# Kernel optimization log

Hardware: AMD Instinct MI355X
Metric: run time of the kernel (lower is better)

The kernel has to match this reference:

```python
import jax, jax.numpy as jnp
import numpy as np

B, C, L = 8, 512, 4096
CK, CV = C // 8, C // 2  # 64, 256


def maxpool2(t):
    # max_pool1d(kernel=2, stride=2) over last axis: [B, c, L] -> [B, c, L//2]
    b, c, l = t.shape
    return t.reshape(b, c, l // 2, 2).max(axis=-1)


def setup_inputs() -> dict:
    key = jax.random.key(0)
    ks = jax.random.split(key, 6)
    return {
        "x": jax.random.normal(ks[0], (B, C, L), dtype=jnp.float32),
        "W_theta": jax.random.normal(ks[1], (CK, C), dtype=jnp.float32) * 0.02,
        "W_phi": jax.random.normal(ks[2], (CK, C), dtype=jnp.float32) * 0.02,
        "W_g": jax.random.normal(ks[3], (CV, C), dtype=jnp.float32) * 0.02,
        "W_o": jax.random.normal(ks[4], (C, CV), dtype=jnp.float32) * 0.02,
        "gamma": jax.random.normal(ks[5], (), dtype=jnp.float32),
    }


def reference(x, W_theta, W_phi, W_g, W_o, gamma):
    # 1x1 convs are channel matmuls
    theta = jnp.einsum("kc,bcl->bkl", W_theta, x)            # [B, C/8, L]
    phi = maxpool2(jnp.einsum("kc,bcl->bkl", W_phi, x))      # [B, C/8, L/2]
    g = maxpool2(jnp.einsum("vc,bcl->bvl", W_g, x))          # [B, C/2, L/2]
    # attention scores over downsampled keys: [B, L, L/2]
    scores = jnp.einsum("bkl,bkm->blm", theta, phi)
    beta = jax.nn.softmax(scores, axis=-1)
    # aggregate values: g @ beta^T -> [B, C/2, L]
    o_in = jnp.einsum("bvm,blm->bvl", g, beta)
    o = jnp.einsum("ov,bvl->bol", W_o, o_in)                 # [B, C, L]
    return gamma * o + x
```

## Files before the change

kernel.cpp:

```cpp
#include <hip/hip_runtime.h>
#include <cstdint>
#include <cstddef>

#define B_ 8
#define C_ 512
#define L_ 4096
#define M_ 2048
#define CK_ 64
#define CV_ 256

typedef _Float16 f16;
typedef _Float16 f16x8 __attribute__((ext_vector_type(8)));
typedef _Float16 f16x4 __attribute__((ext_vector_type(4)));
typedef float f32x4 __attribute__((ext_vector_type(4)));
typedef float f32x16 __attribute__((ext_vector_type(16)));
typedef unsigned int u32x4 __attribute__((ext_vector_type(4)));

#define MFMA16(A, Bv, Cv) __builtin_amdgcn_mfma_f32_16x16x32_f16(A, Bv, Cv, 0, 0, 0)
#define MFMA32(A, Bv, Cv) __builtin_amdgcn_mfma_f32_32x32x16_f16(A, Bv, Cv, 0, 0, 0)

#define LOG2E 1.44269504f

static __device__ __forceinline__ uint32_t pkrtz(float a, float b) {
    return __builtin_bit_cast(uint32_t, __builtin_amdgcn_cvt_pkrtz(a, b));
}

__global__ __launch_bounds__(256) void cvt_all(const float* __restrict__ Wt,
                                               const float* __restrict__ Wp,
                                               const float* __restrict__ Wg,
                                               const float* __restrict__ Wo,
                                               f16* __restrict__ WallF,
                                               f16* __restrict__ WoF) {
    const int i = blockIdx.x * 256 + threadIdx.x;
    const int NW = 384 * 512;
    if (i < NW) {
        const int och = i >> 9, c = i & 511;
        float v;
        if (och < 64)       v = Wt[i];
        else if (och < 128) v = Wp[i - 64 * 512];
        else                v = Wg[i - 128 * 512];
        const int idx = (((och >> 4) * 16 + (c >> 5)) * 64 +
                         (((c >> 3) & 3) << 4) + (och & 15)) * 8 + (c & 7);
        WallF[idx] = (f16)v;
    } else {
        const int j = i - NW;
        const int oc = j >> 8, v = j & 255;
        const int idx = (((oc >> 4) * 8 + (v >> 5)) * 64 +
                         (((v >> 3) & 3) << 4) + (oc & 15)) * 8 + (v & 7);
        WoF[idx] = (f16)Wo[j];
    }
}

__global__ __launch_bounds__(256) void fused_proj(const f16* __restrict__ WallF,
                                                  const float* __restrict__ x,
                                                  f16* __restrict__ theta2,
                                                  f16* __restrict__ phi2,
                                                  f16* __restrict__ g2) {
    __shared__ __align__(16) f16 xs[64][32][8];
    const int b    = blockIdx.y;
    const int l0   = blockIdx.x * 32;
    const int tid  = threadIdx.x;
    const int w    = tid >> 6;
    const int lane = tid & 63;
    const int lq   = lane & 15;
    const int g    = lane >> 4;
    const int wb   = w * 96;

    {
        const float* xb = x + (size_t)b * C_ * L_ + l0 + (tid & 31);
        const int co0 = tid >> 5;
#pragma unroll
        for (int i = 0; i < 8; ++i) {
            const int co = i * 8 + co0;
            float v[8];
#pragma unroll
            for (int j = 0; j < 8; ++j) v[j] = xb[(size_t)(co * 8 + j) * L_];
            u32x4 p = {pkrtz(v[0], v[1]), pkrtz(v[2], v[3]),
                       pkrtz(v[4], v[5]), pkrtz(v[6], v[7])};
            *reinterpret_cast<u32x4*>(&xs[co][tid & 31][0]) = p;
        }
    }
    __syncthreads();

    f32x4 acc[6][2] = {};
    for (int ks = 0; ks < 16; ++ks) {
        f16x8 Bf[2];
#pragma unroll
        for (int lt = 0; lt < 2; ++lt)
            Bf[lt] = *reinterpret_cast<const f16x8*>(&xs[ks * 4 + g][lt * 16 + lq][0]);
#pragma unroll
        for (int t = 0; t < 6; ++t) {
            f16x8 Af = *reinterpret_cast<const f16x8*>(
                WallF + (((size_t)(6 * w + t) * 16 + ks) * 64 + lane) * 8);
            acc[t][0] = MFMA16(Af, Bf[0], acc[t][0]);
            acc[t][1] = MFMA16(Af, Bf[1], acc[t][1]);
        }
    }

#pragma unroll
    for (int t = 0; t < 6; ++t) {
        const int och0 = wb + t * 16;
#pragma unroll
        for (int lt = 0; lt < 2; ++lt) {
            const int l = l0 + lt * 16 + lq;
            if (och0 < 64) {
#pragma unroll
                for (int r = 0; r < 4; ++r) {
                    const int och = och0 + 4 * g + r;
                    theta2[(((size_t)b * 8 + (och >> 3)) * L_ + l) * 8 + (och & 7)] =
                        (f16)(acc[t][lt][r] * LOG2E);
                }
            } else {
#pragma unroll
                for (int r = 0; r < 4; ++r) {
                    const float pv = fmaxf(acc[t][lt][r], __shfl_xor(acc[t][lt][r], 1));
                    if (!(lane & 1)) {
                        const int m = l >> 1;
                        if (och0 < 128) {
                            const int kc = och0 - 64 + 4 * g + r;
                            phi2[(((size_t)b * 8 + (kc >> 3)) * M_ + m) * 8 + (kc & 7)] =
                                (f16)pv;
                        } else {
                            const int vc = och0 - 128 + 4 * g + r;
                            g2[(((size_t)b * 256 + (m >> 3)) * CV_ + vc) * 8 + (m & 7)] =
                                (f16)pv;
                        }
                    }
                }
            }
        }
    }
}

__global__ __launch_bounds__(512, 4) void attn_flash(const f16* __restrict__ theta2,
                                                     const f16* __restrict__ phi2,
                                                     const f16* __restrict__ g2,
                                                     f16* __restrict__ o2) {
    const int bid = blockIdx.x;
    const int b   = bid & 7;
    const int qt  = bid >> 3;
    const int w   = threadIdx.x >> 6;
    const int qg  = w >> 2;
    const int vq  = w & 3;
    const int q0  = qt * 64 + qg * 32;
    const int vb  = vq * 64;
    const int lane = threadIdx.x & 63;
    const int lq   = lane & 31;
    const int hi   = lane >> 5;

    const f16* qbase = theta2 + (size_t)b * 8 * L_ * 8;
    f16x8 Qf[4];
#pragma unroll
    for (int f = 0; f < 4; ++f)
        Qf[f] = *reinterpret_cast<const f16x8*>(
            qbase + ((size_t)(2 * f + hi) * L_ + q0 + lq) * 8);

    f32x16 acc[2] = {};
    float m_run = -3.0e38f;
    float l_run = 0.f;

    const f16* kbase = phi2 + (size_t)b * 8 * M_ * 8;
    const f16* vbase = g2 + (size_t)b * 256 * CV_ * 8;

    uint32_t ko[4], vo[4];
#pragma unroll
    for (int f = 0; f < 4; ++f) ko[f] = ((2 * f + hi) * M_ + lq) * 8u;
#pragma unroll
    for (int ch = 0; ch < 2; ++ch)
#pragma unroll
        for (int vt = 0; vt < 2; ++vt)
            vo[ch * 2 + vt] = ((2 * ch + hi) * CV_ + vb + vt * 32 + lq) * 8u;

    for (int m0 = 0; m0 < M_; m0 += 32) {
        f16x8 Kf[4];
#pragma unroll
        for (int f = 0; f < 4; ++f)
            Kf[f] = *reinterpret_cast<const f16x8*>(kbase + ko[f]);
        f16x8 Vf[2][2];
#pragma unroll
        for (int ch = 0; ch < 2; ++ch)
#pragma unroll
            for (int vt = 0; vt < 2; ++vt)
                Vf[ch][vt] = *reinterpret_cast<const f16x8*>(vbase + vo[ch * 2 + vt]);

        f32x16 S = {};
        __builtin_amdgcn_s_setprio(1);
#pragma unroll
        for (int f = 0; f < 4; ++f) S = MFMA32(Kf[f], Qf[f], S);
        __builtin_amdgcn_s_setprio(0);

        float t0 = fmaxf(fmaxf(S[0], S[1]), S[2]);
        float t1 = fmaxf(fmaxf(S[3], S[4]), S[5]);
        float t2 = fmaxf(fmaxf(S[6], S[7]), S[8]);
        float t3 = fmaxf(fmaxf(S[9], S[10]), S[11]);
        float t4 = fmaxf(fmaxf(S[12], S[13]), S[14]);
        float tm = fmaxf(fmaxf(fmaxf(t0, t1), t2),
                         fmaxf(fmaxf(t3, t4), S[15]));
        tm = fmaxf(tm, __shfl_xor(tm, 32));
        if (__any(tm > m_run + 11.5f)) {
            const float m_new = fmaxf(m_run, tm);
            const float sc = __builtin_amdgcn_exp2f(m_run - m_new);
#pragma unroll
            for (int vt = 0; vt < 2; ++vt)
#pragma unroll
                for (int r = 0; r < 16; ++r) acc[vt][r] *= sc;
            l_run *= sc;
            m_run = m_new;
        }
        float s[16];
#pragma unroll
        for (int r = 0; r < 16; ++r) s[r] = __builtin_amdgcn_exp2f(S[r] - m_run);
        float a0 = (s[0] + s[1]) + (s[2] + s[3]);
        float a1 = (s[4] + s[5]) + (s[6] + s[7]);
        float a2 = (s[8] + s[9]) + (s[10] + s[11]);
        float a3 = (s[12] + s[13]) + (s[14] + s[15]);
        l_run += (a0 + a1) + (a2 + a3);

        uint32_t pk[8];
#pragma unroll
        for (int i = 0; i < 8; ++i) pk[i] = pkrtz(s[2 * i], s[2 * i + 1]);
        asm volatile("v_permlane32_swap_b32 %0, %1" : "+v"(pk[0]), "+v"(pk[2]));
        asm volatile("v_permlane32_swap_b32 %0, %1" : "+v"(pk[1]), "+v"(pk[3]));
        asm volatile("v_permlane32_swap_b32 %0, %1" : "+v"(pk[4]), "+v"(pk[6]));
        asm volatile("v_permlane32_swap_b32 %0, %1" : "+v"(pk[5]), "+v"(pk[7]));
        u32x4 fr0 = {pk[0], pk[1], pk[2], pk[3]};
        u32x4 fr1 = {pk[4], pk[5], pk[6], pk[7]};
        f16x8 P0 = __builtin_bit_cast(f16x8, fr0);
        f16x8 P1 = __builtin_bit_cast(f16x8, fr1);

        __builtin_amdgcn_s_setprio(1);
#pragma unroll
        for (int vt = 0; vt < 2; ++vt) acc[vt] = MFMA32(Vf[0][vt], P0, acc[vt]);
#pragma unroll
        for (int vt = 0; vt < 2; ++vt) acc[vt] = MFMA32(Vf[1][vt], P1, acc[vt]);
        __builtin_amdgcn_s_setprio(0);

#pragma unroll
        for (int f = 0; f < 4; ++f) ko[f] += 32u * 8u;
#pragma unroll
        for (int i = 0; i < 4; ++i) vo[i] += 4u * CV_ * 8u;
    }

    l_run += __shfl_xor(l_run, 32);
    const float inv = 1.f / l_run;
    const int qtile = (q0 >> 4) + (lq >> 4);
    const int ql    = lq & 15;
#pragma unroll
    for (int vt = 0; vt < 2; ++vt)
#pragma unroll
        for (int rq = 0; rq < 4; ++rq) {
            f16x4 o;
#pragma unroll
            for (int j = 0; j < 4; ++j) o[j] = (f16)(acc[vt][4 * rq + j] * inv);
            f16* p = o2 + ((((size_t)b * 256 + qtile) * 8 + vq * 2 + vt) * 64 +
                           rq * 16 + ql) * 8 + 4 * hi;
            *reinterpret_cast<f16x4*>(p) = o;
        }
}

__global__ __launch_bounds__(256) void out_mfma(const f16* __restrict__ WoF,
                                                const f16* __restrict__ o2,
                                                const float* __restrict__ x,
                                                const float* __restrict__ gamma_p,
                                                float* __restrict__ out) {
    const int b    = blockIdx.z;
    const int l0   = blockIdx.x * 64;
    const int wid  = threadIdx.x >> 6;
    const int oc0  = blockIdx.y * 64 + wid * 16;
    const int lane = threadIdx.x & 63;
    const int lq   = lane & 15;
    const int g    = lane >> 4;

    f32x4 acc[4] = {{0.f, 0.f, 0.f, 0.f}, {0.f, 0.f, 0.f, 0.f},
                    {0.f, 0.f, 0.f, 0.f}, {0.f, 0.f, 0.f, 0.f}};
#pragma unroll
    for (int ks = 0; ks < 8; ++ks) {
        f16x8 A = *reinterpret_cast<const f16x8*>(
            WoF + (((size_t)(oc0 >> 4) * 8 + ks) * 64 + lane) * 8);
#pragma unroll
        for (int lt = 0; lt < 4; ++lt) {
            const f16* bp = o2 + (((size_t)(b * 256 + (l0 >> 4) + lt) * 8 + ks) * 64 +
                                  lane) * 8;
            acc[lt] = MFMA16(A, *reinterpret_cast<const f16x8*>(bp), acc[lt]);
        }
    }
    const float gamma = *gamma_p;
#pragma unroll
    for (int lt = 0; lt < 4; ++lt)
#pragma unroll
        for (int r = 0; r < 4; ++r) {
            const size_t o = ((size_t)b * C_ + oc0 + 4 * g + r) * L_ + l0 + lt * 16 + lq;
            out[o] = fmaf(gamma, acc[lt][r], x[o]);
        }
}

extern "C" void kernel_launch(void* const* d_in, const int* in_sizes, int n_in,
                              void* d_out, int out_size, void* d_ws, size_t ws_size,
                              hipStream_t stream) {
    const float* x       = (const float*)d_in[0];
    const float* W_theta = (const float*)d_in[1];
    const float* W_phi   = (const float*)d_in[2];
    const float* W_g     = (const float*)d_in[3];
    const float* W_o     = (const float*)d_in[4];
    const float* gamma   = (const float*)d_in[5];
    float* out = (float*)d_out;

    f16* theta2 = (f16*)d_ws;
    f16* phi2   = theta2 + (size_t)B_ * 8 * L_ * 8;
    f16* g2     = phi2 + (size_t)B_ * 8 * M_ * 8;
    f16* o2     = g2 + (size_t)B_ * 256 * CV_ * 8;
    f16* WoF    = o2 + (size_t)B_ * L_ * CV_;
    f16* WallF  = WoF + (size_t)C_ * CV_;

    const int cvt_n = 384 * 512 + 512 * 256;
    cvt_all<<<dim3(cvt_n / 256), 256, 0, stream>>>(W_theta, W_phi, W_g, W_o, WallF, WoF);
    fused_proj<<<dim3(L_ / 32, B_), 256, 0, stream>>>(WallF, x, theta2, phi2, g2);
    attn_flash<<<dim3(512), 512, 0, stream>>>(theta2, phi2, g2, o2);
    out_mfma<<<dim3(L_ / 64, C_ / 64, B_), 256, 0, stream>>>(WoF, o2, x, gamma, out);
}
```

Baseline: 176.9 us.

## Split attention key range across wave pairs and merge partial softmax via LDS

```diff
diff --git a/kernel.cpp b/kernel.cpp
--- a/kernel.cpp
+++ b/kernel.cpp
@@ -12,6 +12,7 @@
 typedef _Float16 f16;
 typedef _Float16 f16x8 __attribute__((ext_vector_type(8)));
 typedef _Float16 f16x4 __attribute__((ext_vector_type(4)));
+typedef _Float16 f16x2 __attribute__((ext_vector_type(2)));
 typedef float f32x4 __attribute__((ext_vector_type(4)));
 typedef float f32x16 __attribute__((ext_vector_type(16)));
 typedef unsigned int u32x4 __attribute__((ext_vector_type(4)));
@@ -136,14 +137,17 @@
                                                      const f16* __restrict__ phi2,
                                                      const f16* __restrict__ g2,
                                                      f16* __restrict__ o2) {
+    __shared__ uint32_t lds_o[2][2][64][33];
+    __shared__ float lds_ml[2][2][2][64];
     const int bid = blockIdx.x;
     const int b   = bid & 7;
     const int qt  = bid >> 3;
     const int w   = threadIdx.x >> 6;
     const int qg  = w >> 2;
-    const int vq  = w & 3;
+    const int vq  = (w >> 1) & 1;
+    const int mh  = w & 1;
     const int q0  = qt * 64 + qg * 32;
-    const int vb  = vq * 64;
+    const int vb  = vq * 128;
     const int lane = threadIdx.x & 63;
     const int lq   = lane & 31;
     const int hi   = lane >> 5;
@@ -155,33 +159,32 @@
         Qf[f] = *reinterpret_cast<const f16x8*>(
             qbase + ((size_t)(2 * f + hi) * L_ + q0 + lq) * 8);
 
-    f32x16 acc[2] = {};
+    f32x16 acc[4] = {};
     float m_run = -3.0e38f;
     float l_run = 0.f;
 
     const f16* kbase = phi2 + (size_t)b * 8 * M_ * 8;
     const f16* vbase = g2 + (size_t)b * 256 * CV_ * 8;
 
-    uint32_t ko[4], vo[4];
-#pragma unroll
-    for (int f = 0; f < 4; ++f) ko[f] = ((2 * f + hi) * M_ + lq) * 8u;
+    uint32_t ko[4], vo[2];
+#pragma unroll
+    for (int f = 0; f < 4; ++f) ko[f] = ((2 * f + hi) * M_ + mh * 1024 + lq) * 8u;
 #pragma unroll
     for (int ch = 0; ch < 2; ++ch)
-#pragma unroll
-        for (int vt = 0; vt < 2; ++vt)
-            vo[ch * 2 + vt] = ((2 * ch + hi) * CV_ + vb + vt * 32 + lq) * 8u;
-
-    for (int m0 = 0; m0 < M_; m0 += 32) {
+        vo[ch] = ((mh * 128 + 2 * ch + hi) * CV_ + vb + lq) * 8u;
+
+    for (int it = 0; it < 32; ++it) {
         f16x8 Kf[4];
 #pragma unroll
         for (int f = 0; f < 4; ++f)
             Kf[f] = *reinterpret_cast<const f16x8*>(kbase + ko[f]);
-        f16x8 Vf[2][2];
+        f16x8 Vf[2][4];
 #pragma unroll
         for (int ch = 0; ch < 2; ++ch)
 #pragma unroll
-            for (int vt = 0; vt < 2; ++vt)
-                Vf[ch][vt] = *reinterpret_cast<const f16x8*>(vbase + vo[ch * 2 + vt]);
+            for (int vt = 0; vt < 4; ++vt)
+                Vf[ch][vt] = *reinterpret_cast<const f16x8*>(
+                    vbase + vo[ch] + vt * 32 * 8);
 
         f32x16 S = {};
         __builtin_amdgcn_s_setprio(1);
@@ -201,7 +204,7 @@
             const float m_new = fmaxf(m_run, tm);
             const float sc = __builtin_amdgcn_exp2f(m_run - m_new);
 #pragma unroll
-            for (int vt = 0; vt < 2; ++vt)
+            for (int vt = 0; vt < 4; ++vt)
 #pragma unroll
                 for (int r = 0; r < 16; ++r) acc[vt][r] *= sc;
             l_run *= sc;
@@ -230,32 +233,60 @@
 
         __builtin_amdgcn_s_setprio(1);
 #pragma unroll
-        for (int vt = 0; vt < 2; ++vt) acc[vt] = MFMA32(Vf[0][vt], P0, acc[vt]);
-#pragma unroll
-        for (int vt = 0; vt < 2; ++vt) acc[vt] = MFMA32(Vf[1][vt], P1, acc[vt]);
+        for (int vt = 0; vt < 4; ++vt) acc[vt] = MFMA32(Vf[0][vt], P0, acc[vt]);
+#pragma unroll
+        for (int vt = 0; vt < 4; ++vt) acc[vt] = MFMA32(Vf[1][vt], P1, acc[vt]);
         __builtin_amdgcn_s_setprio(0);
 
 #pragma unroll
         for (int f = 0; f < 4; ++f) ko[f] += 32u * 8u;
-#pragma unroll
-        for (int i = 0; i < 4; ++i) vo[i] += 4u * CV_ * 8u;
-    }
-
-    l_run += __shfl_xor(l_run, 32);
-    const float inv = 1.f / l_run;
-    const int qtile = (q0 >> 4) + (lq >> 4);
-    const int ql    = lq & 15;
-#pragma unroll
-    for (int vt = 0; vt < 2; ++vt)
-#pragma unroll
-        for (int rq = 0; rq < 4; ++rq) {
-            f16x4 o;
-#pragma unroll
-            for (int j = 0; j < 4; ++j) o[j] = (f16)(acc[vt][4 * rq + j] * inv);
-            f16* p = o2 + ((((size_t)b * 256 + qtile) * 8 + vq * 2 + vt) * 64 +
-                           rq * 16 + ql) * 8 + 4 * hi;
-            *reinterpret_cast<f16x4*>(p) = o;
-        }
+        vo[0] += 4u * CV_ * 8u;
+        vo[1] += 4u * CV_ * 8u;
+    }
+
+    const float l_full = l_run + __shfl_xor(l_run, 32);
+
+    if (mh == 1) {
+        const float inv = 1.f / l_full;
+#pragma unroll
+        for (int t = 0; t < 32; ++t) {
+            const int vt = t >> 3, r2 = (t & 7) * 2;
+            lds_o[qg][vq][lane][t] = pkrtz(acc[vt][r2] * inv, acc[vt][r2 + 1] * inv);
+        }
+        lds_ml[qg][vq][0][lane] = m_run;
+        lds_ml[qg][vq][1][lane] = l_full;
+    }
+    __syncthreads();
+    if (mh == 0) {
+        const float mB = lds_ml[qg][vq][0][lane];
+        const float lB = lds_ml[qg][vq][1][lane];
+        const float ms = fmaxf(m_run, mB);
+        const float wA = __builtin_amdgcn_exp2f(m_run - ms) * l_full;
+        const float wB = __builtin_amdgcn_exp2f(mB - ms) * lB;
+        const float denom = wA + wB;
+        const float aA = wA / (denom * l_full);
+        const float aB = wB / denom;
+
+        const int qtile = (q0 >> 4) + (lq >> 4);
+        const int ql    = lq & 15;
+#pragma unroll
+        for (int vt = 0; vt < 4; ++vt)
+#pragma unroll
+            for (int rq = 0; rq < 4; ++rq) {
+                f16x4 o;
+#pragma unroll
+                for (int jp = 0; jp < 2; ++jp) {
+                    const uint32_t pb = lds_o[qg][vq][lane][vt * 8 + rq * 2 + jp];
+                    const f16x2 hb = __builtin_bit_cast(f16x2, pb);
+                    const int r = rq * 4 + jp * 2;
+                    o[jp * 2]     = (f16)(acc[vt][r] * aA + (float)hb[0] * aB);
+                    o[jp * 2 + 1] = (f16)(acc[vt][r + 1] * aA + (float)hb[1] * aB);
+                }
+                f16* p = o2 + ((((size_t)b * 256 + qtile) * 8 + vq * 4 + vt) * 64 +
+                               rq * 16 + ql) * 8 + 4 * hi;
+                *reinterpret_cast<f16x4*>(p) = o;
+            }
+    }
 }
 
 __global__ __launch_bounds__(256) void out_mfma(const f16* __restrict__ WoF,
```

Measured after the change: 282.2 us. +59.5%, slower.

## Split attention key range in two with a separate log-sum-exp combine kernel

Applied to the files above, without the earlier changes.

```diff
diff --git a/kernel.cpp b/kernel.cpp
--- a/kernel.cpp
+++ b/kernel.cpp
@@ -135,8 +135,11 @@
 __global__ __launch_bounds__(512, 4) void attn_flash(const f16* __restrict__ theta2,
                                                      const f16* __restrict__ phi2,
                                                      const f16* __restrict__ g2,
-                                                     f16* __restrict__ o2) {
+                                                     f16* __restrict__ op,
+                                                     float* __restrict__ mlm,
+                                                     float* __restrict__ mll) {
     const int bid = blockIdx.x;
+    const int mh  = blockIdx.y;
     const int b   = bid & 7;
     const int qt  = bid >> 3;
     const int w   = threadIdx.x >> 6;
@@ -164,14 +167,14 @@
 
     uint32_t ko[4], vo[4];
 #pragma unroll
-    for (int f = 0; f < 4; ++f) ko[f] = ((2 * f + hi) * M_ + lq) * 8u;
+    for (int f = 0; f < 4; ++f) ko[f] = ((2 * f + hi) * M_ + mh * 1024 + lq) * 8u;
 #pragma unroll
     for (int ch = 0; ch < 2; ++ch)
 #pragma unroll
         for (int vt = 0; vt < 2; ++vt)
-            vo[ch * 2 + vt] = ((2 * ch + hi) * CV_ + vb + vt * 32 + lq) * 8u;
-
-    for (int m0 = 0; m0 < M_; m0 += 32) {
+            vo[ch * 2 + vt] = ((mh * 128 + 2 * ch + hi) * CV_ + vb + vt * 32 + lq) * 8u;
+
+    for (int it = 0; it < 32; ++it) {
         f16x8 Kf[4];
 #pragma unroll
         for (int f = 0; f < 4; ++f)
@@ -241,10 +244,11 @@
         for (int i = 0; i < 4; ++i) vo[i] += 4u * CV_ * 8u;
     }
 
-    l_run += __shfl_xor(l_run, 32);
-    const float inv = 1.f / l_run;
+    const float l_full = l_run + __shfl_xor(l_run, 32);
+    const float inv = 1.f / l_full;
     const int qtile = (q0 >> 4) + (lq >> 4);
     const int ql    = lq & 15;
+    f16* opm = op + (size_t)mh * B_ * L_ * CV_;
 #pragma unroll
     for (int vt = 0; vt < 2; ++vt)
 #pragma unroll
@@ -252,10 +256,42 @@
             f16x4 o;
 #pragma unroll
             for (int j = 0; j < 4; ++j) o[j] = (f16)(acc[vt][4 * rq + j] * inv);
-            f16* p = o2 + ((((size_t)b * 256 + qtile) * 8 + vq * 2 + vt) * 64 +
-                           rq * 16 + ql) * 8 + 4 * hi;
+            f16* p = opm + ((((size_t)b * 256 + qtile) * 8 + vq * 2 + vt) * 64 +
+                            rq * 16 + ql) * 8 + 4 * hi;
             *reinterpret_cast<f16x4*>(p) = o;
         }
+    if (vq == 0 && hi == 0) {
+        const int q = q0 + lq;
+        mlm[(size_t)mh * B_ * L_ + (size_t)b * L_ + q] = m_run;
+        mll[(size_t)mh * B_ * L_ + (size_t)b * L_ + q] = l_full;
+    }
+}
+
+__global__ __launch_bounds__(256) void combine(const f16* __restrict__ opA,
+                                               const f16* __restrict__ opB,
+                                               const float* __restrict__ mlm,
+                                               const float* __restrict__ mll,
+                                               f16* __restrict__ o2) {
+    const int c = blockIdx.x * 256 + threadIdx.x;
+    const int lane  = c & 63;
+    const int qtile = (c >> 9) & 255;
+    const int b     = c >> 17;
+    const int q     = qtile * 16 + (lane & 15);
+    const size_t mi = (size_t)b * L_ + q;
+    const float mA = mlm[mi],            lA = mll[mi];
+    const float mB = mlm[B_ * L_ + mi],  lB = mll[B_ * L_ + mi];
+    const float ms = fmaxf(mA, mB);
+    const float wA = __builtin_amdgcn_exp2f(mA - ms) * lA;
+    const float wB = __builtin_amdgcn_exp2f(mB - ms) * lB;
+    const float d  = wA + wB;
+    const float aA = wA / d, aB = wB / d;
+    const f16x8 va = *reinterpret_cast<const f16x8*>(opA + (size_t)c * 8);
+    const f16x8 vb = *reinterpret_cast<const f16x8*>(opB + (size_t)c * 8);
+    f16x8 o;
+#pragma unroll
+    for (int j = 0; j < 8; ++j)
+        o[j] = (f16)((float)va[j] * aA + (float)vb[j] * aB);
+    *reinterpret_cast<f16x8*>(o2 + (size_t)c * 8) = o;
 }
 
 __global__ __launch_bounds__(256) void out_mfma(const f16* __restrict__ WoF,
@@ -308,13 +344,18 @@
     f16* theta2 = (f16*)d_ws;
     f16* phi2   = theta2 + (size_t)B_ * 8 * L_ * 8;
     f16* g2     = phi2 + (size_t)B_ * 8 * M_ * 8;
-    f16* o2     = g2 + (size_t)B_ * 256 * CV_ * 8;
-    f16* WoF    = o2 + (size_t)B_ * L_ * CV_;
+    f16* op     = g2 + (size_t)B_ * 256 * CV_ * 8;
+    f16* o2     = op;
+    f16* WoF    = op + (size_t)2 * B_ * L_ * CV_;
     f16* WallF  = WoF + (size_t)C_ * CV_;
+    float* mlm  = (float*)(WallF + (size_t)384 * C_);
+    float* mll  = mlm + (size_t)2 * B_ * L_;
 
     const int cvt_n = 384 * 512 + 512 * 256;
     cvt_all<<<dim3(cvt_n / 256), 256, 0, stream>>>(W_theta, W_phi, W_g, W_o, WallF, WoF);
     fused_proj<<<dim3(L_ / 32, B_), 256, 0, stream>>>(WallF, x, theta2, phi2, g2);
-    attn_flash<<<dim3(512), 512, 0, stream>>>(theta2, phi2, g2, o2);
+    attn_flash<<<dim3(512, 2), 512, 0, stream>>>(theta2, phi2, g2, op, mlm, mll);
+    combine<<<dim3((B_ * L_ * CV_ / 8) / 256), 256, 0, stream>>>(
+        op, op + (size_t)B_ * L_ * CV_, mlm, mll, o2);
     out_mfma<<<dim3(L_ / 64, C_ / 64, B_), 256, 0, stream>>>(WoF, o2, x, gamma, out);
 }
```

Measured after the change: 187.0 us. +5.7%, slower.
